# Kernel optimization log

Hardware: AMD Instinct MI355X
Metric: run time of the kernel (lower is better)

## Reference

```python
import jax, jax.numpy as jnp
import numpy as np

B, L, D = 2, 256, 256  # batch, length, raw feature dim (W dims are D+1)

def setup_inputs() -> dict:
    key = jax.random.key(0)
    k1, k2, k3, kw = jax.random.split(key, 4)
    layer1 = jax.random.normal(k1, (B, L, D), dtype=jnp.float32)
    layer2 = jax.random.normal(k2, (B, L, D), dtype=jnp.float32)
    layer3 = jax.random.normal(k3, (B, L, D), dtype=jnp.float32)
    # xavier_normal_ for a 3D tensor: fan_in = D+1 * (D+1) receptive? torch treats
    # dim0 as fan_out-ish; we just use a matched-scale gaussian (correctness of the
    # contraction math is what matters for the kernel baseline).
    std = float(np.sqrt(2.0 / ((D + 1) + (D + 1) * (D + 1))))
    W = jax.random.normal(kw, (D + 1, D + 1, D + 1), dtype=jnp.float32) * std
    return {"layer1": layer1, "layer2": layer2, "layer3": layer3, "W": W}

def _append_ones(x):
    ones = jnp.ones(x.shape[:2] + (1,), dtype=x.dtype)
    return jnp.concatenate([x, ones], axis=-1)

def reference(layer1, layer2, layer3, W):
    l1 = _append_ones(layer1)  # [n, L, a]
    l2 = _append_ones(layer2)  # [n, L, b]
    l3 = _append_ones(layer3)  # [n, L, c]
    # Chained contraction: nia,abc -> nibc ; nibc,njb -> nijc ; nijc,nkc -> nijk
    t = jnp.einsum('nia,abc->nibc', l1, W)
    t = jnp.einsum('nibc,njb->nijc', t, l2)
    out = jnp.einsum('nijc,nkc->nijk', t, l3)
    return out
```

## Files before the change

### kernel.cpp

```cpp
#include <hip/hip_runtime.h>

typedef unsigned short u16;
typedef __attribute__((ext_vector_type(8))) short bf16x8;
typedef __attribute__((ext_vector_type(4))) float f32x4;

#define GLOAD_LDS16(gsrc, ldst)                                               \
  __builtin_amdgcn_global_load_lds(                                           \
      (const __attribute__((address_space(1))) void*)(gsrc),                  \
      (__attribute__((address_space(3))) void*)(ldst), 16, 0, 0)

#define LDSOFF(p) \
  ((unsigned)(uintptr_t)(__attribute__((address_space(3))) const void*)(p))

#define SB0 __builtin_amdgcn_sched_barrier(0)

__device__ __forceinline__ u16 f2bf(float x) {
  unsigned u = __float_as_uint(x);
  u = (u + 0x7FFFu + ((u >> 16) & 1u)) >> 16;
  return (u16)u;
}

__global__ void prep_l_kernel(const float* __restrict__ l1,
                              const float* __restrict__ l2,
                              const float* __restrict__ l3,
                              u16* __restrict__ o1, u16* __restrict__ o2,
                              u16* __restrict__ o3) {
  int idx = blockIdx.x * 256 + threadIdx.x;
  const int NR = 512 * 288;
  if (idx >= 3 * NR) return;
  int which = idx / NR, rem = idx - which * NR;
  int r = rem / 288, p = rem - r * 288;
  const float* s = which == 0 ? l1 : which == 1 ? l2 : l3;
  u16* d = which == 0 ? o1 : which == 1 ? o2 : o3;
  float v = (p < 256) ? s[r * 256 + p] : (p == 256 ? 1.0f : 0.0f);
  d[rem] = f2bf(v);
}

__global__ __launch_bounds__(256, 4) void prep_w_kernel(
    const float* __restrict__ W, u16* __restrict__ W2) {
  __shared__ float tf[64][65];
  const int a0 = blockIdx.x * 64, c0 = blockIdx.y * 64, b = blockIdx.z;
  const int t = threadIdx.x;
  const bool bok = (b < 257);

  float v[16];
#pragma unroll
  for (int i = 0; i < 16; ++i) {
    int idx = t + i * 256;
    int ar = idx >> 6, cc = idx & 63;
    int a = a0 + ar, c = c0 + cc;
    v[i] = (bok && a < 257 && c < 257) ? W[((long)a * 257 + b) * 257 + c] : 0.0f;
  }
#pragma unroll
  for (int i = 0; i < 16; ++i) {
    int idx = t + i * 256;
    int ar = idx >> 6, cc = idx & 63;
    tf[cc][ar] = v[i];
  }
  __syncthreads();

#pragma unroll
  for (int p = 0; p < 2; ++p) {
    int q = t + p * 256;
    int cr = q >> 3, ach = q & 7;
    int c = c0 + cr;
    int abase = a0 + ach * 8;
    if (c < 288 && abase < 288) {
      u16 pk[8];
#pragma unroll
      for (int j = 0; j < 8; ++j) pk[j] = f2bf(tf[cr][ach * 8 + j]);
      *(uint4*)(&W2[((long)c * 288 + b) * 288 + abase]) = *(uint4*)pk;
    }
  }
}

__global__ __launch_bounds__(256, 3) void gemm_nt(
    const u16* __restrict__ A, const u16* __restrict__ B, u16* __restrict__ C,
    int K, int lda, int ldb, int ldc) {
  __shared__ u16 As[2][4096];
  __shared__ u16 Bs[2][4096];
  const int t = threadIdx.x;
  const int bid = blockIdx.x;
  const int xcd = bid & 7, s = bid >> 3;
  const int nt = xcd * 81 + (s >> 2);
  const int mt = s & 3;
  const int m0 = mt * 128, n0 = nt * 128;
  const int lane = t & 63;
  const int w = t >> 6;
  const int wr = (w >> 1) * 64, wc = (w & 1) * 64;
  const int r16 = lane & 15;
  const int cgrp = lane >> 4;
  const int rr = cgrp * 4;
  const unsigned ABase = LDSOFF(&As[0][0]);
  const unsigned BBase = LDSOFF(&Bs[0][0]);
  (void)K;

  const u16* PA = A + (long)m0 * lda;
  const u16* PB = B + (long)n0 * ldb;

#define STG(buf, k0)                                                          \
  {                                                                           \
    _Pragma("unroll") for (int _p = 0; _p < 2; ++_p) {                        \
      int _q = t + _p * 256;                                                  \
      int _r = _q >> 2, _g = (_q & 3) ^ ((_r >> 1) & 3);                      \
      GLOAD_LDS16(PA + (long)_r * lda + (k0) + _g * 8, &As[buf][_q * 8]);     \
      GLOAD_LDS16(PB + (long)_r * ldb + (k0) + _g * 8, &Bs[buf][_q * 8]);     \
    }                                                                         \
  }

  f32x4 acc[4][4];
  const f32x4 zero = {0.f, 0.f, 0.f, 0.f};
#pragma unroll
  for (int i = 0; i < 4; ++i)
#pragma unroll
    for (int j = 0; j < 4; ++j) acc[i][j] = zero;

  STG(0, 0);

#define GCOL(NI)                                                              \
  __builtin_amdgcn_s_setprio(1);                                              \
  _Pragma("unroll") for (int _mi = 0; _mi < 4; ++_mi)                         \
    acc[_mi][NI] = __builtin_amdgcn_mfma_f32_16x16x32_bf16(                   \
        af[_mi], bf[NI], acc[_mi][NI], 0, 0, 0);                              \
  __builtin_amdgcn_s_setprio(0);                                              \
  SB0;

#define GSTEP(KS)                                                             \
  {                                                                           \
    asm volatile("s_waitcnt vmcnt(0)" ::: "memory");                          \
    SB0;                                                                      \
    __builtin_amdgcn_s_barrier();                                             \
    SB0;                                                                      \
    bf16x8 af[4], bf[4];                                                      \
    _Pragma("unroll") for (int mi = 0; mi < 4; ++mi) {                        \
      int R = wr + mi * 16 + r16;                                             \
      unsigned ao = ABase + (unsigned)(((((KS) & 1) * 4096) + R * 32 +        \
                                       ((cgrp ^ ((R >> 1) & 3)) * 8)) * 2);   \
      asm volatile("ds_read_b128 %0, %1" : "=v"(af[mi]) : "v"(ao));           \
    }                                                                         \
    _Pragma("unroll") for (int ni = 0; ni < 4; ++ni) {                        \
      int R = wc + ni * 16 + r16;                                             \
      unsigned ao = BBase + (unsigned)(((((KS) & 1) * 4096) + R * 32 +        \
                                       ((cgrp ^ ((R >> 1) & 3)) * 8)) * 2);   \
      asm volatile("ds_read_b128 %0, %1" : "=v"(bf[ni]) : "v"(ao));           \
    }                                                                         \
    SB0;                                                                      \
    if ((KS) < 8) STG(((KS) + 1) & 1, ((KS) + 1) * 32);                       \
    SB0;                                                                      \
    asm volatile("s_waitcnt lgkmcnt(3)" ::: "memory"); SB0;                   \
    GCOL(0)                                                                   \
    asm volatile("s_waitcnt lgkmcnt(2)" ::: "memory"); SB0;                   \
    GCOL(1)                                                                   \
    asm volatile("s_waitcnt lgkmcnt(1)" ::: "memory"); SB0;                   \
    GCOL(2)                                                                   \
    asm volatile("s_waitcnt lgkmcnt(0)" ::: "memory"); SB0;                   \
    GCOL(3)                                                                   \
  }

  GSTEP(0) GSTEP(1) GSTEP(2) GSTEP(3) GSTEP(4)
  GSTEP(5) GSTEP(6) GSTEP(7) GSTEP(8)
#undef GSTEP
#undef GCOL
#undef STG

#pragma unroll
  for (int mi = 0; mi < 4; ++mi) {
    int gm = m0 + wr + mi * 16 + rr;
#pragma unroll
    for (int ni = 0; ni < 4; ++ni) {
      int gc = n0 + wc + ni * 16 + r16;
#pragma unroll
      for (int r = 0; r < 4; ++r)
        C[(long)(gm + r) * ldc + gc] = f2bf(acc[mi][ni][r]);
    }
  }
}

__global__ __launch_bounds__(256, 2) void fused23(
    const u16* __restrict__ l2b, const u16* __restrict__ l3b,
    const u16* __restrict__ T1, float* __restrict__ out) {
  __shared__ u16 S[64 * 296];
  __shared__ u16 Bst[2][288 * 32];
  const int t = threadIdx.x;
  const int lane = t & 63;
  const int w = t >> 6;

  const int bid = blockIdx.x;
  const int xcd = bid & 7;
  const int seq = bid >> 3;
  const int ni = xcd * 64 + (seq >> 2);
  const int q = seq & 3;
  const int n = ni >> 8;

  const int r16 = lane & 15;
  const int cgrp = lane >> 4;
  const int kb = cgrp * 8;
  const int rr = cgrp * 4;
  const f32x4 zero = {0.f, 0.f, 0.f, 0.f};

  const u16* A2 = l2b + (long)n * 73728 + (long)(q * 64) * 288;
  const u16* BT = T1 + (long)ni * 82944;
  const u16* B3 = l3b + (long)n * 73728;
  const unsigned BOF = LDSOFF(&Bst[0][0]);
  const unsigned SOF = LDSOFF(&S[0]);

#define ISSUE_A(buf, kk)                                                      \
  {                                                                           \
    _Pragma("unroll") for (int _p = 0; _p < 5; ++_p) {                        \
      int _q = t + _p * 256;                                                  \
      if (_q < 1152) {                                                        \
        int _r = _q >> 2, _g = (_q & 3) ^ ((_r >> 1) & 3);                    \
        GLOAD_LDS16(BT + (long)_r * 288 + (kk) * 32 + _g * 8,                 \
                    &Bst[(buf)][_q * 8]);                                     \
      }                                                                       \
    }                                                                         \
  }
#define ISSUE_B(buf, kk)                                                      \
  {                                                                           \
    _Pragma("unroll") for (int _p = 0; _p < 4; ++_p) {                        \
      int _q = t + _p * 256;                                                  \
      int _r = _q >> 2, _g = (_q & 3) ^ ((_r >> 1) & 3);                      \
      GLOAD_LDS16(B3 + (long)_r * 288 + (kk) * 32 + _g * 8,                   \
                  &Bst[(buf)][_q * 8]);                                       \
    }                                                                         \
  }

  {
    const int wm = w & 1, wn = w >> 1;
    f32x4 acc[2][9];
#pragma unroll
    for (int i = 0; i < 2; ++i)
#pragma unroll
      for (int j = 0; j < 9; ++j) acc[i][j] = zero;

    ISSUE_A(0, 0);

    bf16x8 afr[18];
#pragma unroll
    for (int k = 0; k < 9; ++k)
#pragma unroll
      for (int mi = 0; mi < 2; ++mi)
        afr[k * 2 + mi] = *(const bf16x8*)(A2 +
            (long)(wm * 32 + mi * 16 + r16) * 288 + k * 32 + kb);
    SB0;

#define FA_MM(NJ)                                                             \
  __builtin_amdgcn_s_setprio(1);                                              \
  acc[0][NJ] = __builtin_amdgcn_mfma_f32_16x16x32_bf16(afc0, bf[NJ], acc[0][NJ], 0, 0, 0); \
  acc[1][NJ] = __builtin_amdgcn_mfma_f32_16x16x32_bf16(afc1, bf[NJ], acc[1][NJ], 0, 0, 0); \
  __builtin_amdgcn_s_setprio(0);

#define FA_STEP(K)                                                            \
  {                                                                           \
    asm volatile("s_waitcnt vmcnt(0)" ::: "memory");                          \
    SB0;                                                                      \
    __builtin_amdgcn_s_barrier();                                             \
    SB0;                                                                      \
    bf16x8 bf[9];                                                             \
    _Pragma("unroll") for (int nj = 0; nj < 9; ++nj) {                        \
      const int R = wn * 144 + nj * 16 + r16;                                 \
      unsigned ao = BOF + (unsigned)((((K) & 1) * 9216 + R * 32 +             \
                                      ((cgrp ^ ((R >> 1) & 3)) * 8)) * 2);    \
      asm volatile("ds_read_b128 %0, %1" : "=v"(bf[nj]) : "v"(ao));           \
    }                                                                         \
    SB0;                                                                      \
    if ((K) < 8) ISSUE_A(((K) + 1) & 1, (K) + 1);                             \
    SB0;                                                                      \
    const bf16x8 afc0 = afr[(K) * 2 + 0], afc1 = afr[(K) * 2 + 1];            \
    asm volatile("s_waitcnt lgkmcnt(6)" ::: "memory"); SB0;                   \
    FA_MM(0) FA_MM(1) FA_MM(2) SB0;                                           \
    asm volatile("s_waitcnt lgkmcnt(3)" ::: "memory"); SB0;                   \
    FA_MM(3) FA_MM(4) FA_MM(5) SB0;                                           \
    asm volatile("s_waitcnt lgkmcnt(0)" ::: "memory"); SB0;                   \
    FA_MM(6) FA_MM(7) FA_MM(8) SB0;                                           \
  }
    FA_STEP(0) FA_STEP(1) FA_STEP(2) FA_STEP(3) FA_STEP(4)
    FA_STEP(5) FA_STEP(6) FA_STEP(7) FA_STEP(8)
#undef FA_STEP
#undef FA_MM

    __syncthreads();
    ISSUE_B(0, 0);
#pragma unroll
    for (int mi = 0; mi < 2; ++mi)
#pragma unroll
      for (int nj = 0; nj < 9; ++nj)
#pragma unroll
        for (int qq = 0; qq < 4; ++qq)
          S[(wm * 32 + mi * 16 + rr + qq) * 296 + wn * 144 + nj * 16 + r16] =
              f2bf(acc[mi][nj][qq]);
  }
  __syncthreads();

  {
    f32x4 acc[4][4];
#pragma unroll
    for (int i = 0; i < 4; ++i)
#pragma unroll
      for (int j = 0; j < 4; ++j) acc[i][j] = zero;

#define FB_MM(NI)                                                             \
  __builtin_amdgcn_s_setprio(1);                                              \
  _Pragma("unroll") for (int _mi = 0; _mi < 4; ++_mi)                         \
    acc[_mi][NI] = __builtin_amdgcn_mfma_f32_16x16x32_bf16(                   \
        af[_mi], bf[NI], acc[_mi][NI], 0, 0, 0);                              \
  __builtin_amdgcn_s_setprio(0);                                              \
  SB0;

#define FB_STEP(K)                                                            \
  {                                                                           \
    asm volatile("s_waitcnt vmcnt(0)" ::: "memory");                          \
    SB0;                                                                      \
    __builtin_amdgcn_s_barrier();                                             \
    SB0;                                                                      \
    bf16x8 af[4], bf[4];                                                      \
    _Pragma("unroll") for (int mi = 0; mi < 4; ++mi) {                        \
      unsigned ao = SOF + (unsigned)(((mi * 16 + r16) * 296 +                 \
                                      (K) * 32 + kb) * 2);                    \
      asm volatile("ds_read_b128 %0, %1" : "=v"(af[mi]) : "v"(ao));           \
    }                                                                         \
    _Pragma("unroll") for (int nj = 0; nj < 4; ++nj) {                        \
      const int R = w * 64 + nj * 16 + r16;                                   \
      unsigned ao = BOF + (unsigned)((((K) & 1) * 9216 + R * 32 +             \
                                      ((cgrp ^ ((R >> 1) & 3)) * 8)) * 2);    \
      asm volatile("ds_read_b128 %0, %1" : "=v"(bf[nj]) : "v"(ao));           \
    }                                                                         \
    SB0;                                                                      \
    if ((K) < 8) ISSUE_B(((K) + 1) & 1, (K) + 1);                             \
    SB0;                                                                      \
    asm volatile("s_waitcnt lgkmcnt(3)" ::: "memory"); SB0;                   \
    FB_MM(0)                                                                  \
    asm volatile("s_waitcnt lgkmcnt(2)" ::: "memory"); SB0;                   \
    FB_MM(1)                                                                  \
    asm volatile("s_waitcnt lgkmcnt(1)" ::: "memory"); SB0;                   \
    FB_MM(2)                                                                  \
    asm volatile("s_waitcnt lgkmcnt(0)" ::: "memory"); SB0;                   \
    FB_MM(3)                                                                  \
  }
    FB_STEP(0) FB_STEP(1) FB_STEP(2) FB_STEP(3) FB_STEP(4)
    FB_STEP(5) FB_STEP(6) FB_STEP(7) FB_STEP(8)
#undef FB_STEP
#undef FB_MM

    float* O = out + (long)ni * 65536 + (long)(q * 64) * 256 + w * 64;
#pragma unroll
    for (int mi = 0; mi < 4; ++mi)
#pragma unroll
      for (int nj = 0; nj < 4; ++nj)
#pragma unroll
        for (int qq = 0; qq < 4; ++qq)
          O[(long)(mi * 16 + rr + qq) * 256 + nj * 16 + r16] = acc[mi][nj][qq];
  }
#undef ISSUE_A
#undef ISSUE_B
}

extern "C" void kernel_launch(void* const* d_in, const int* in_sizes, int n_in,
                              void* d_out, int out_size, void* d_ws, size_t ws_size,
                              hipStream_t stream) {
  const float* l1 = (const float*)d_in[0];
  const float* l2 = (const float*)d_in[1];
  const float* l3 = (const float*)d_in[2];
  const float* W = (const float*)d_in[3];
  float* out = (float*)d_out;
  char* ws = (char*)d_ws;

  const long LB = 512L * 288 * 2;
  u16* l1b = (u16*)ws;
  u16* l2b = (u16*)(ws + LB);
  u16* l3b = (u16*)(ws + 2 * LB);
  u16* T1 = (u16*)(ws + 3 * LB);
  u16* W2 = (u16*)d_out;

  prep_l_kernel<<<1728, 256, 0, stream>>>(l1, l2, l3, l1b, l2b, l3b);

  dim3 gw(5, 5, 288);
  prep_w_kernel<<<gw, 256, 0, stream>>>(W, W2);

  gemm_nt<<<2592, 256, 0, stream>>>(l1b, W2, T1, 288, 288, 288, 82944);

  fused23<<<2048, 256, 0, stream>>>(l2b, l3b, T1, out);
}
```

Before: 148.3 us.

## Split fused23 work across 512 threads with per-step A-fragment loads

The fused second/third contraction kernel now runs 8 waves per block instead of 4. Each wave computes a smaller output tile in both phases, and the cooperative global-to-LDS loads are spread over more threads. The A fragments of l2 are no longer preloaded for all k-steps (18 registers); they are double-buffered and loaded one step ahead. This lowers register pressure and raises latency hiding, at the cost of more barrier participants and less per-wave reuse of the B fragments read from LDS.

```diff
diff --git a/kernel.cpp b/kernel.cpp
--- a/kernel.cpp
+++ b/kernel.cpp
@@ -176,7 +176,7 @@
   }
 }
 
-__global__ __launch_bounds__(256, 2) void fused23(
+__global__ __launch_bounds__(512, 4) void fused23(
     const u16* __restrict__ l2b, const u16* __restrict__ l3b,
     const u16* __restrict__ T1, float* __restrict__ out) {
   __shared__ u16 S[64 * 296];
@@ -206,8 +206,8 @@
 
 #define ISSUE_A(buf, kk)                                                      \
   {                                                                           \
-    _Pragma("unroll") for (int _p = 0; _p < 5; ++_p) {                        \
-      int _q = t + _p * 256;                                                  \
+    _Pragma("unroll") for (int _p = 0; _p < 3; ++_p) {                        \
+      int _q = t + _p * 512;                                                  \
       if (_q < 1152) {                                                        \
         int _r = _q >> 2, _g = (_q & 3) ^ ((_r >> 1) & 3);                    \
         GLOAD_LDS16(BT + (long)_r * 288 + (kk) * 32 + _g * 8,                 \
@@ -217,8 +217,8 @@
   }
 #define ISSUE_B(buf, kk)                                                      \
   {                                                                           \
-    _Pragma("unroll") for (int _p = 0; _p < 4; ++_p) {                        \
-      int _q = t + _p * 256;                                                  \
+    _Pragma("unroll") for (int _p = 0; _p < 2; ++_p) {                        \
+      int _q = t + _p * 512;                                                  \
       int _r = _q >> 2, _g = (_q & 3) ^ ((_r >> 1) & 3);                      \
       GLOAD_LDS16(B3 + (long)_r * 288 + (kk) * 32 + _g * 8,                   \
                   &Bst[(buf)][_q * 8]);                                       \
@@ -226,84 +226,79 @@
   }
 
   {
-    const int wm = w & 1, wn = w >> 1;
-    f32x4 acc[2][9];
-#pragma unroll
-    for (int i = 0; i < 2; ++i)
-#pragma unroll
-      for (int j = 0; j < 9; ++j) acc[i][j] = zero;
+    const int wj = w & 3, wc2 = w >> 2;
+    const u16* Ap = A2 + (long)(wj * 16 + r16) * 288 + kb;
+    f32x4 acc[9];
+#pragma unroll
+    for (int j = 0; j < 9; ++j) acc[j] = zero;
 
     ISSUE_A(0, 0);
-
-    bf16x8 afr[18];
-#pragma unroll
-    for (int k = 0; k < 9; ++k)
-#pragma unroll
-      for (int mi = 0; mi < 2; ++mi)
-        afr[k * 2 + mi] = *(const bf16x8*)(A2 +
-            (long)(wm * 32 + mi * 16 + r16) * 288 + k * 32 + kb);
+    bf16x8 afrA = *(const bf16x8*)(Ap);
+    bf16x8 afrB;
     SB0;
 
-#define FA_MM(NJ)                                                             \
+#define FA_MM(NJ, AFC)                                                        \
   __builtin_amdgcn_s_setprio(1);                                              \
-  acc[0][NJ] = __builtin_amdgcn_mfma_f32_16x16x32_bf16(afc0, bf[NJ], acc[0][NJ], 0, 0, 0); \
-  acc[1][NJ] = __builtin_amdgcn_mfma_f32_16x16x32_bf16(afc1, bf[NJ], acc[1][NJ], 0, 0, 0); \
+  acc[NJ] = __builtin_amdgcn_mfma_f32_16x16x32_bf16(AFC, bf[NJ], acc[NJ], 0, 0, 0); \
   __builtin_amdgcn_s_setprio(0);
 
-#define FA_STEP(K)                                                            \
+#define FA_STEP(K, AFC, AFN)                                                  \
   {                                                                           \
     asm volatile("s_waitcnt vmcnt(0)" ::: "memory");                          \
     SB0;                                                                      \
     __builtin_amdgcn_s_barrier();                                             \
+    SB0;                                                                      \
+    if ((K) < 8) {                                                            \
+      ISSUE_A(((K) + 1) & 1, (K) + 1);                                        \
+      AFN = *(const bf16x8*)(Ap + ((K) + 1) * 32);                            \
+    }                                                                         \
     SB0;                                                                      \
     bf16x8 bf[9];                                                             \
     _Pragma("unroll") for (int nj = 0; nj < 9; ++nj) {                        \
-      const int R = wn * 144 + nj * 16 + r16;                                 \
+      const int R = wc2 * 144 + nj * 16 + r16;                                \
       unsigned ao = BOF + (unsigned)((((K) & 1) * 9216 + R * 32 +             \
                                       ((cgrp ^ ((R >> 1) & 3)) * 8)) * 2);    \
       asm volatile("ds_read_b128 %0, %1" : "=v"(bf[nj]) : "v"(ao));           \
     }                                                                         \
     SB0;                                                                      \
-    if ((K) < 8) ISSUE_A(((K) + 1) & 1, (K) + 1);                             \
-    SB0;                                                                      \
-    const bf16x8 afc0 = afr[(K) * 2 + 0], afc1 = afr[(K) * 2 + 1];            \
     asm volatile("s_waitcnt lgkmcnt(6)" ::: "memory"); SB0;                   \
-    FA_MM(0) FA_MM(1) FA_MM(2) SB0;                                           \
+    FA_MM(0, AFC) FA_MM(1, AFC) FA_MM(2, AFC) SB0;                            \
     asm volatile("s_waitcnt lgkmcnt(3)" ::: "memory"); SB0;                   \
-    FA_MM(3) FA_MM(4) FA_MM(5) SB0;                                           \
+    FA_MM(3, AFC) FA_MM(4, AFC) FA_MM(5, AFC) SB0;                            \
     asm volatile("s_waitcnt lgkmcnt(0)" ::: "memory"); SB0;                   \
-    FA_MM(6) FA_MM(7) FA_MM(8) SB0;                                           \
-  }
-    FA_STEP(0) FA_STEP(1) FA_STEP(2) FA_STEP(3) FA_STEP(4)
-    FA_STEP(5) FA_STEP(6) FA_STEP(7) FA_STEP(8)
+    FA_MM(6, AFC) FA_MM(7, AFC) FA_MM(8, AFC) SB0;                            \
+  }
+    FA_STEP(0, afrA, afrB) FA_STEP(1, afrB, afrA)
+    FA_STEP(2, afrA, afrB) FA_STEP(3, afrB, afrA)
+    FA_STEP(4, afrA, afrB) FA_STEP(5, afrB, afrA)
+    FA_STEP(6, afrA, afrB) FA_STEP(7, afrB, afrA)
+    FA_STEP(8, afrA, afrB)
 #undef FA_STEP
 #undef FA_MM
 
     __syncthreads();
     ISSUE_B(0, 0);
 #pragma unroll
-    for (int mi = 0; mi < 2; ++mi)
-#pragma unroll
-      for (int nj = 0; nj < 9; ++nj)
-#pragma unroll
-        for (int qq = 0; qq < 4; ++qq)
-          S[(wm * 32 + mi * 16 + rr + qq) * 296 + wn * 144 + nj * 16 + r16] =
-              f2bf(acc[mi][nj][qq]);
+    for (int nj = 0; nj < 9; ++nj)
+#pragma unroll
+      for (int qq = 0; qq < 4; ++qq)
+        S[(wj * 16 + rr + qq) * 296 + wc2 * 144 + nj * 16 + r16] =
+            f2bf(acc[nj][qq]);
   }
   __syncthreads();
 
   {
-    f32x4 acc[4][4];
-#pragma unroll
-    for (int i = 0; i < 4; ++i)
+    const int wjb = w & 1, wk = w >> 1;
+    f32x4 acc[2][4];
+#pragma unroll
+    for (int i = 0; i < 2; ++i)
 #pragma unroll
       for (int j = 0; j < 4; ++j) acc[i][j] = zero;
 
 #define FB_MM(NI)                                                             \
   __builtin_amdgcn_s_setprio(1);                                              \
-  _Pragma("unroll") for (int _mi = 0; _mi < 4; ++_mi)                         \
-    acc[_mi][NI] = __builtin_amdgcn_mfma_f32_16x16x32_bf16(                   \
-        af[_mi], bf[NI], acc[_mi][NI], 0, 0, 0);                              \
+  acc[0][NI] = __builtin_amdgcn_mfma_f32_16x16x32_bf16(af[0], bf[NI], acc[0][NI], 0, 0, 0); \
+  acc[1][NI] = __builtin_amdgcn_mfma_f32_16x16x32_bf16(af[1], bf[NI], acc[1][NI], 0, 0, 0); \
   __builtin_amdgcn_s_setprio(0);                                              \
   SB0;
 
@@ -313,20 +308,20 @@
     SB0;                                                                      \
     __builtin_amdgcn_s_barrier();                                             \
     SB0;                                                                      \
-    bf16x8 af[4], bf[4];                                                      \
-    _Pragma("unroll") for (int mi = 0; mi < 4; ++mi) {                        \
-      unsigned ao = SOF + (unsigned)(((mi * 16 + r16) * 296 +                 \
+    if ((K) < 8) ISSUE_B(((K) + 1) & 1, (K) + 1);                             \
+    SB0;                                                                      \
+    bf16x8 af[2], bf[4];                                                      \
+    _Pragma("unroll") for (int mi = 0; mi < 2; ++mi) {                        \
+      unsigned ao = SOF + (unsigned)(((wjb * 32 + mi * 16 + r16) * 296 +      \
                                       (K) * 32 + kb) * 2);                    \
       asm volatile("ds_read_b128 %0, %1" : "=v"(af[mi]) : "v"(ao));           \
     }                                                                         \
     _Pragma("unroll") for (int nj = 0; nj < 4; ++nj) {                        \
-      const int R = w * 64 + nj * 16 + r16;                                   \
+      const int R = wk * 64 + nj * 16 + r16;                                  \
       unsigned ao = BOF + (unsigned)((((K) & 1) * 9216 + R * 32 +             \
                                       ((cgrp ^ ((R >> 1) & 3)) * 8)) * 2);    \
       asm volatile("ds_read_b128 %0, %1" : "=v"(bf[nj]) : "v"(ao));           \
     }                                                                         \
-    SB0;                                                                      \
-    if ((K) < 8) ISSUE_B(((K) + 1) & 1, (K) + 1);                             \
     SB0;                                                                      \
     asm volatile("s_waitcnt lgkmcnt(3)" ::: "memory"); SB0;                   \
     FB_MM(0)                                                                  \
@@ -342,9 +337,9 @@
 #undef FB_STEP
 #undef FB_MM
 
-    float* O = out + (long)ni * 65536 + (long)(q * 64) * 256 + w * 64;
-#pragma unroll
-    for (int mi = 0; mi < 4; ++mi)
+    float* O = out + (long)ni * 65536 + (long)(q * 64 + wjb * 32) * 256 + wk * 64;
+#pragma unroll
+    for (int mi = 0; mi < 2; ++mi)
 #pragma unroll
       for (int nj = 0; nj < 4; ++nj)
 #pragma unroll
@@ -379,5 +374,5 @@
 
   gemm_nt<<<2592, 256, 0, stream>>>(l1b, W2, T1, 288, 288, 288, 82944);
 
-  fused23<<<2048, 256, 0, stream>>>(l2b, l3b, T1, out);
-}
+  fused23<<<2048, 512, 0, stream>>>(l2b, l3b, T1, out);
+}
```

Measured after the change: 146.3 us. No clear change (-1.3%).
